# Performance work log

Measured on AMD Instinct MI355X. Metric: run time of the kernel, lower is better.

## Reference

```python
import jax, jax.numpy as jnp
import numpy as np

N_NODES = 50000
N_EDGES = 600000
D = 128


def setup_inputs() -> dict:
    key = jax.random.key(0)
    ks = jax.random.split(key, 10)
    feat = jax.random.normal(ks[0], (N_NODES, D), dtype=jnp.float32)
    edge_src = jax.random.randint(ks[1], (N_EDGES,), 0, N_NODES, dtype=jnp.int64)
    edge_dst = jax.random.randint(ks[2], (N_EDGES,), 0, N_NODES, dtype=jnp.int64)
    edge_w = jax.random.uniform(ks[3], (N_EDGES,), dtype=jnp.float32)
    s = 1.0 / np.sqrt(D)
    W1 = jax.random.uniform(ks[4], (D, D), minval=-s, maxval=s, dtype=jnp.float32)
    W2 = jax.random.uniform(ks[5], (D, D), minval=-s, maxval=s, dtype=jnp.float32)
    # torch GRUCell params: weight_ih [3H, 2D], weight_hh [3H, H], biases [3H]
    W_ih = jax.random.uniform(ks[6], (3 * D, 2 * D), minval=-s, maxval=s, dtype=jnp.float32)
    W_hh = jax.random.uniform(ks[7], (3 * D, D), minval=-s, maxval=s, dtype=jnp.float32)
    b_ih = jax.random.uniform(ks[8], (3 * D,), minval=-s, maxval=s, dtype=jnp.float32)
    b_hh = jax.random.uniform(ks[9], (3 * D,), minval=-s, maxval=s, dtype=jnp.float32)
    return {"feat": feat, "edge_src": edge_src, "edge_dst": edge_dst, "edge_w": edge_w,
            "W1": W1, "W2": W2, "W_ih": W_ih, "W_hh": W_hh, "b_ih": b_ih, "b_hh": b_hh}


def _weighted_mean_agg(feat, w, src, dst, n_nodes):
    # message: ft[src] * w; reduce: sum(m) / sum(w) per dst node (zero for isolated nodes)
    m = feat[src] * w[:, None]                                   # [E, D]
    sm = jax.ops.segment_sum(m, dst, num_segments=n_nodes)      # [N, D]
    sw = jax.ops.segment_sum(w, dst, num_segments=n_nodes)      # [N]
    has = sw > 0
    denom = jnp.where(has, sw, 1.0)[:, None]
    return jnp.where(has[:, None], sm / denom, 0.0)


def reference(feat, edge_src, edge_dst, edge_w, W1, W2, W_ih, W_hh, b_ih, b_hh):
    n = feat.shape[0]
    neigh1 = _weighted_mean_agg(feat, edge_w, edge_src, edge_dst, n)  # forward graph
    neigh2 = _weighted_mean_agg(feat, edge_w, edge_dst, edge_src, n)  # reverse graph
    hn = jnp.concatenate([neigh1 @ W1.T, neigh2 @ W2.T], axis=1)      # [N, 2D]
    # torch.nn.GRUCell(hn, feat)
    gi = hn @ W_ih.T + b_ih    # [N, 3D]
    gh = feat @ W_hh.T + b_hh  # [N, 3D]
    ir, iz, inn = jnp.split(gi, 3, axis=1)
    hr, hz, hnn = jnp.split(gh, 3, axis=1)
    r = jax.nn.sigmoid(ir + hr)
    z = jax.nn.sigmoid(iz + hz)
    ng = jnp.tanh(inn + r * hnn)
    return (1.0 - z) * ng + z * feat
```

## Files before the change

kernel.cpp:

```cpp
#include <hip/hip_runtime.h>
#include <math.h>

#define N_NODES 50000
#define N_EDGES 600000
#define D 128
#define KTOT 384
#define NCOLS 512

#define SCAN_CHUNK 512
#define SCAN_NB ((N_NODES + SCAN_CHUNK - 1) / SCAN_CHUNK)

#define GEMM_ROWB ((N_NODES + 127) / 128)
#define GEMM_NWG  (GEMM_ROWB * 8)
#define NXCD 8
#define KHALF 192

#define BSHIFT 10
#define NBUCKETS ((N_NODES + (1 << BSHIFT) - 1) >> BSHIFT)
#define PA_NB 512
#define PA_CHUNK ((N_EDGES + PA_NB - 1) / PA_NB)
#define PB_SPLIT 4

typedef unsigned int u32;
typedef unsigned short u16;

typedef __attribute__((ext_vector_type(8))) short bf16x8;
typedef __attribute__((ext_vector_type(4))) float f32x4;

__device__ __forceinline__ float bits2f(u32 u) {
    float f; __builtin_memcpy(&f, &u, 4);
    return f;
}
__device__ __forceinline__ u16 f2b(float f) {
    u32 u; __builtin_memcpy(&u, &f, 4);
    u32 r = (u + 0x7fffu + ((u >> 16) & 1u)) >> 16;
    return (u16)r;
}

__global__ void fill_sentinel(float* __restrict__ p, long n, float v) {
    long i = (long)blockIdx.x * blockDim.x + threadIdx.x;
    long stride = (long)gridDim.x * blockDim.x;
    for (; i < n; i += stride) p[i] = v;
}

__global__ void front(const float* __restrict__ feat, u16* __restrict__ fb16,
                      u32* __restrict__ offz) {
    long stride = (long)gridDim.x * blockDim.x;
    long t0 = (long)blockIdx.x * blockDim.x + threadIdx.x;
    for (long i = t0; i < 2 * N_NODES; i += stride) offz[i] = 0u;
    for (long i = t0; i < (long)N_NODES * (D / 4); i += stride) {
        int n = (int)(i >> 5), j4 = (int)(i & 31);
        float4 v = *(const float4*)(feat + (size_t)n * D + j4 * 4);
        ushort4 o;
        o.x = f2b(v.x); o.y = f2b(v.y); o.z = f2b(v.z); o.w = f2b(v.w);
        *(ushort4*)(fb16 + ((size_t)n << 7) + j4 * 4) = o;
    }
}

__global__ void count_both(const int* __restrict__ esrc, const int* __restrict__ edst,
                           int* __restrict__ cnt1, int* __restrict__ cnt2) {
    int e = blockIdx.x * blockDim.x + threadIdx.x;
    if (e < N_EDGES) {
        atomicAdd(&cnt1[edst[e]], 1);
        atomicAdd(&cnt2[esrc[e]], 1);
    }
}

__global__ void scan_partial(const int* __restrict__ off, int* __restrict__ bsum) {
    int dir = blockIdx.y, bx = blockIdx.x, t = threadIdx.x;
    const int* a = off + (size_t)dir * N_NODES;
    int i0 = bx * SCAN_CHUNK + 2 * t;
    int s = 0;
    if (i0 < N_NODES) s += a[i0];
    if (i0 + 1 < N_NODES) s += a[i0 + 1];
    __shared__ int red[256];
    red[t] = s;
    __syncthreads();
    for (int d = 128; d > 0; d >>= 1) {
        if (t < d) red[t] += red[t + d];
        __syncthreads();
    }
    if (t == 0) bsum[dir * SCAN_NB + bx] = red[0];
}

__global__ void scan_bsums(int* __restrict__ bsum) {
    __shared__ int part[256];
    int t = threadIdx.x;
    int i = t & 127, dir = t >> 7;
    int v = (i < SCAN_NB) ? bsum[dir * SCAN_NB + i] : 0;
    part[t] = v;
    __syncthreads();
    for (int d = 1; d < 128; d <<= 1) {
        int add = (i >= d) ? part[t - d] : 0;
        __syncthreads();
        part[t] += add;
        __syncthreads();
    }
    if (i < SCAN_NB) bsum[dir * SCAN_NB + i] = part[t] - v;
}

__global__ void scan_final(int* __restrict__ off, const int* __restrict__ bsum) {
    int dir = blockIdx.y, bx = blockIdx.x, t = threadIdx.x;
    int* a = off + (size_t)dir * N_NODES;
    int base = bsum[dir * SCAN_NB + bx];
    int i0 = bx * SCAN_CHUNK + 2 * t;
    int e0 = (i0 < N_NODES) ? a[i0] : 0;
    int e1 = (i0 + 1 < N_NODES) ? a[i0 + 1] : 0;
    __shared__ int part[256];
    int v = e0 + e1;
    part[t] = v;
    __syncthreads();
    for (int d = 1; d < 256; d <<= 1) {
        int add = (t >= d) ? part[t - d] : 0;
        __syncthreads();
        part[t] += add;
        __syncthreads();
    }
    int tb = base + part[t] - v;
    if (i0 < N_NODES) a[i0] = tb;
    if (i0 + 1 < N_NODES) a[i0 + 1] = tb + e0;
}

__global__ void init_buckets(const int* __restrict__ off1, const int* __restrict__ off2,
                             int* __restrict__ bks) {
    int t = threadIdx.x;
    if (t <= NBUCKETS) {
        int n = t << BSHIFT;
        int s1 = (t == NBUCKETS) ? N_EDGES : off1[n];
        int s2 = (t == NBUCKETS) ? N_EDGES : off2[n];
        bks[t] = s1;
        bks[128 + t] = s2;
        if (t < NBUCKETS) { bks[64 + t] = s1; bks[192 + t] = s2; }
    }
}

__global__ __launch_bounds__(256)
void partA(const int* __restrict__ esrc, const int* __restrict__ edst,
           const float* __restrict__ ew, int* __restrict__ bks,
           uint2* __restrict__ tmp1, uint2* __restrict__ tmp2) {
    __shared__ int lcnt[NBUCKETS];
    __shared__ int lbase[NBUCKETS + 1];
    __shared__ int gbase[NBUCKETS];
    __shared__ uint2 stage[PA_CHUNK];
    int dir = blockIdx.y;
    const int* key = dir ? esrc : edst;
    const int* nbr = dir ? edst : esrc;
    int* bucketFill = bks + (dir ? 192 : 64);
    uint2* tmp = dir ? tmp2 : tmp1;

    int t = threadIdx.x;
    int e0 = blockIdx.x * PA_CHUNK;
    int e1 = min(e0 + PA_CHUNK, N_EDGES);
    if (t < NBUCKETS) lcnt[t] = 0;
    __syncthreads();
    for (int e = e0 + t; e < e1; e += 256)
        atomicAdd(&lcnt[key[e] >> BSHIFT], 1);
    __syncthreads();
    if (t == 0) {
        int s = 0;
        for (int b = 0; b < NBUCKETS; ++b) { lbase[b] = s; s += lcnt[b]; }
        lbase[NBUCKETS] = s;
    }
    __syncthreads();
    if (t < NBUCKETS) {
        gbase[t] = atomicAdd(&bucketFill[t], lcnt[t]);
        lcnt[t] = 0;
    }
    __syncthreads();
    for (int e = e0 + t; e < e1; e += 256) {
        int k = key[e];
        int b = k >> BSHIFT;
        int i = lbase[b] + atomicAdd(&lcnt[b], 1);
        u32 wb = (u32)f2b(ew[e]);
        stage[i] = make_uint2(((u32)k << 16) | (u32)nbr[e], ((u32)b << 16) | wb);
    }
    __syncthreads();
    int total = lbase[NBUCKETS];
    for (int i = t; i < total; i += 256) {
        uint2 v = stage[i];
        int b = (int)(v.y >> 16);
        tmp[gbase[b] + (i - lbase[b])] = make_uint2(v.x, v.y & 0xffffu);
    }
}

__global__ __launch_bounds__(256)
void partB(const uint2* __restrict__ tmp1, const uint2* __restrict__ tmp2,
           const int* __restrict__ bks,
           int* __restrict__ off1, int* __restrict__ off2,
           u32* __restrict__ csr1, u32* __restrict__ csr2) {
    int dir = blockIdx.z;
    const uint2* tmp = dir ? tmp2 : tmp1;
    const int* bucketStart = bks + dir * 128;
    int* off = dir ? off2 : off1;
    u32* csr = dir ? csr2 : csr1;

    int b = blockIdx.x;
    int s = bucketStart[b], e = bucketStart[b + 1];
    int cnt = e - s;
    int per = (cnt + PB_SPLIT - 1) / PB_SPLIT;
    int ss = s + blockIdx.y * per;
    int ee = min(ss + per, e);
    for (int i = ss + (int)threadIdx.x; i < ee; i += 256) {
        uint2 v = tmp[i];
        int dst = v.x >> 16;
        int p = atomicAdd(&off[dst], 1);
        csr[p] = ((v.x & 0xffffu) << 16) | (v.y & 0xffffu);
    }
}

__global__ void gather_both(u16* __restrict__ Ah2, const u16* __restrict__ fb16,
                            const int* __restrict__ off1, const u32* __restrict__ csr1,
                            const int* __restrict__ off2, const u32* __restrict__ csr2) {
    int gw = (blockIdx.x * blockDim.x + threadIdx.x) >> 6;
    int lane = threadIdx.x & 63;
    if (gw >= 2 * N_NODES) return;
    int dir = (gw >= N_NODES);
    int n = dir ? gw - N_NODES : gw;
    const int* off = dir ? off2 : off1;
    const u32* csr = dir ? csr2 : csr1;
    int start = (n == 0) ? 0 : off[n - 1];
    int end = off[n];
    int half = lane >> 5;
    int hl = lane & 31;
    const u16* fbl = fb16 + hl * 4;
    float a0 = 0.f, a1 = 0.f, a2 = 0.f, a3 = 0.f, sw = 0.f;
    int p = start;
    for (; p + 3 < end; p += 4) {
        u32 cA = csr[p + half];
        u32 cB = csr[p + 2 + half];
        uint2 vA = *(const uint2*)(fbl + ((size_t)(cA >> 16) << 7));
        uint2 vB = *(const uint2*)(fbl + ((size_t)(cB >> 16) << 7));
        float wA = bits2f(cA << 16), wB = bits2f(cB << 16);
        a0 += bits2f(vA.x << 16) * wA + bits2f(vB.x << 16) * wB;
        a1 += bits2f(vA.x & 0xffff0000u) * wA + bits2f(vB.x & 0xffff0000u) * wB;
        a2 += bits2f(vA.y << 16) * wA + bits2f(vB.y << 16) * wB;
        a3 += bits2f(vA.y & 0xffff0000u) * wA + bits2f(vB.y & 0xffff0000u) * wB;
        sw += wA + wB;
    }
    for (; p < end; p += 2) {
        u32 c = (p + half < end) ? csr[p + half] : 0u;
        uint2 v = *(const uint2*)(fbl + ((size_t)(c >> 16) << 7));
        float w = bits2f(c << 16);
        a0 += bits2f(v.x << 16) * w;
        a1 += bits2f(v.x & 0xffff0000u) * w;
        a2 += bits2f(v.y << 16) * w;
        a3 += bits2f(v.y & 0xffff0000u) * w;
        sw += w;
    }
    a0 += __shfl_xor(a0, 32);
    a1 += __shfl_xor(a1, 32);
    a2 += __shfl_xor(a2, 32);
    a3 += __shfl_xor(a3, 32);
    sw += __shfl_xor(sw, 32);
    if (lane < 32) {
        float inv = (sw > 0.f) ? 1.f / sw : 0.f;
        if (!isfinite(inv)) inv = 0.f;
        uint2 o;
        o.x = ((u32)f2b(a1 * inv) << 16) | (u32)f2b(a0 * inv);
        o.y = ((u32)f2b(a3 * inv) << 16) | (u32)f2b(a2 * inv);
        *(uint2*)(Ah2 + ((size_t)n << 8) + dir * 128 + hl * 4) = o;
    }
}

__global__ void compute_M(const float* __restrict__ W_ih,
                          const float* __restrict__ W1,
                          const float* __restrict__ W2,
                          float* __restrict__ M1, float* __restrict__ M2) {
    int r = blockIdx.x;
    int k = threadIdx.x;
    int which = blockIdx.y;
    const float* Wsel = which ? W2 : W1;
    const float* ih = W_ih + (size_t)r * (2 * D) + which * D;
    float acc = 0.f;
    for (int j = 0; j < D; ++j) acc += ih[j] * Wsel[j * D + k];
    (which ? M2 : M1)[r * D + k] = acc;
}

__global__ void fill_Bt(const float* __restrict__ M1, const float* __restrict__ M2,
                        const float* __restrict__ W_hh, u16* __restrict__ Bt) {
    int idx = blockIdx.x * blockDim.x + threadIdx.x;
    if (idx >= NCOLS * KTOT) return;
    int cp = idx / KTOT;
    int k  = idx - cp * KTOT;
    int c = cp >> 2, g = cp & 3;
    float v = 0.f;
    if (g <= 1) {
        int r = c + (g == 1 ? 128 : 0);
        v = (k < 128) ? M1[r * D + k]
          : (k < 256) ? M2[r * D + (k - 128)]
                      : W_hh[r * D + (k - 256)];
    } else if (g == 2) {
        int r = c + 256;
        v = (k < 128) ? M1[r * D + k]
          : (k < 256) ? M2[r * D + (k - 128)] : 0.f;
    } else {
        v = (k >= 256) ? W_hh[(c + 256) * D + (k - 256)] : 0.f;
    }
    if (!isfinite(v)) v = 0.f;
    Bt[idx] = f2b(v);
}

#define LOAD_A(m, k) ((k) < 8 ? *(const bf16x8*)(aP[m] + (k) * 32) \
                              : *(const bf16x8*)(fP[m] + ((k) - 8) * 32))

__global__ __launch_bounds__(256)
void gemm_gru_mfma(const u16* __restrict__ Ah2, const u16* __restrict__ fb16,
                   const u16* __restrict__ Bt, const float* __restrict__ feat,
                   const float* __restrict__ b_ih, const float* __restrict__ b_hh,
                   float* __restrict__ out) {
    __shared__ __align__(16) char smem[64 * KHALF * 2];
    float (*epi)[16][65] = (float(*)[16][65])smem;

    int bid = blockIdx.x;
    int wgid = (bid % NXCD) * (GEMM_NWG / NXCD) + bid / NXCD;
    int rowp = wgid >> 3;
    int colb = wgid & 7;
    int tid = threadIdx.x, lane = tid & 63, wid = tid >> 6;
    int mw = rowp * 128 + wid * 32;
    int nw = colb * 64;
    int rif = lane & 15, kg = lane >> 4;

    int scol = tid >> 2;
    int sq   = tid & 3;
    u32 sbase = (u32)scol * (KHALF * 2) + (u32)sq * 96;
    u32 sxor  = (u32)((scol & 7) << 4);
    const u16* ssrc0 = Bt + (size_t)(nw + scol) * KTOT + sq * 48;

    u32 bCol[4], bXor[4];
    #pragma unroll
    for (int n = 0; n < 4; ++n) {
        u32 col = n * 16 + rif;
        bCol[n] = col * (KHALF * 2) + kg * 16;
        bXor[n] = (col & 7) << 4;
    }

    f32x4 acc[2][4];
    #pragma unroll
    for (int m = 0; m < 2; ++m)
        #pragma unroll
        for (int n = 0; n < 4; ++n)
            acc[m][n] = (f32x4){0.f, 0.f, 0.f, 0.f};

    const u16* aP[2];
    const u16* fP[2];
    #pragma unroll
    for (int m = 0; m < 2; ++m) {
        int arow = min(mw + m * 16 + rif, N_NODES - 1);
        aP[m] = Ah2 + ((size_t)arow << 8) + kg * 8;
        fP[m] = fb16 + ((size_t)arow << 7) + kg * 8;
    }

    #pragma unroll
    for (int i = 0; i < 6; ++i) {
        bf16x8 v = *(const bf16x8*)(ssrc0 + i * 8);
        *(bf16x8*)(smem + ((sbase + i * 16) ^ sxor)) = v;
    }

    bf16x8 abuf[4][2];
    #pragma unroll
    for (int s = 0; s < 3; ++s)
        #pragma unroll
        for (int m = 0; m < 2; ++m)
            abuf[s][m] = LOAD_A(m, s);

    __syncthreads();

    #pragma unroll
    for (int ks = 0; ks < 6; ++ks) {
        if (ks + 3 < KTOT / 32) {
            #pragma unroll
            for (int m = 0; m < 2; ++m)
                abuf[(ks + 3) & 3][m] = LOAD_A(m, ks + 3);
        }
        bf16x8 bfr[4];
        #pragma unroll
        for (int n = 0; n < 4; ++n)
            bfr[n] = *(const bf16x8*)(smem + ((bCol[n] + ks * 64) ^ bXor[n]));
        #pragma unroll
        for (int m = 0; m < 2; ++m)
            #pragma unroll
            for (int n = 0; n < 4; ++n)
                acc[m][n] = __builtin_amdgcn_mfma_f32_16x16x32_bf16(
                    abuf[ks & 3][m], bfr[n], acc[m][n], 0, 0, 0);
    }

    __syncthreads();

    #pragma unroll
    for (int i = 0; i < 6; ++i) {
        bf16x8 v = *(const bf16x8*)(ssrc0 + KHALF + i * 8);
        *(bf16x8*)(smem + ((sbase + i * 16) ^ sxor)) = v;
    }
    __syncthreads();

    #pragma unroll
    for (int ks = 6; ks < 12; ++ks) {
        if (ks + 3 < KTOT / 32) {
            #pragma unroll
            for (int m = 0; m < 2; ++m)
                abuf[(ks + 3) & 3][m] = LOAD_A(m, ks + 3);
        }
        bf16x8 bfr[4];
        #pragma unroll
        for (int n = 0; n < 4; ++n)
            bfr[n] = *(const bf16x8*)(smem + ((bCol[n] + (ks - 6) * 64) ^ bXor[n]));
        #pragma unroll
        for (int m = 0; m < 2; ++m)
            #pragma unroll
            for (int n = 0; n < 4; ++n)
                acc[m][n] = __builtin_amdgcn_mfma_f32_16x16x32_bf16(
                    abuf[ks & 3][m], bfr[n], acc[m][n], 0, 0, 0);
    }

    int rc0 = nw >> 2;
    int erow = lane >> 2;
    int g4 = lane & 3;
    int cbase = rc0 + g4 * 4;
    float4 bi_r = *(const float4*)(b_ih + cbase);
    float4 bh_r = *(const float4*)(b_hh + cbase);
    float4 bi_z = *(const float4*)(b_ih + cbase + 128);
    float4 bh_z = *(const float4*)(b_hh + cbase + 128);
    float4 bi_n = *(const float4*)(b_ih + cbase + 256);
    float4 bh_n = *(const float4*)(b_hh + cbase + 256);

    #pragma unroll
    for (int m = 0; m < 2; ++m) {
        __syncthreads();
        #pragma unroll
        for (int n = 0; n < 4; ++n)
            #pragma unroll
            for (int reg = 0; reg < 4; ++reg)
                epi[wid][kg * 4 + reg][n * 16 + rif] = acc[m][n][reg];
        __syncthreads();

        float4 q0 = *(const float4*)&epi[wid][erow][g4 * 16 + 0];
        float4 q1 = *(const float4*)&epi[wid][erow][g4 * 16 + 4];
        float4 q2 = *(const float4*)&epi[wid][erow][g4 * 16 + 8];
        float4 q3 = *(const float4*)&epi[wid][erow][g4 * 16 + 12];

        int node = mw + m * 16 + erow;
        if (node < N_NODES) {
            float4 f = *(const float4*)(feat + (size_t)node * D + cbase);
            float4 res;
            {
                float r = 1.f / (1.f + __expf(-(q0.x + bi_r.x + bh_r.x)));
                float z = 1.f / (1.f + __expf(-(q0.y + bi_z.x + bh_z.x)));
                float ng = tanhf(q0.z + bi_n.x + r * (q0.w + bh_n.x));
                res.x = (1.f - z) * ng + z * f.x;
            }
            {
                float r = 1.f / (1.f + __expf(-(q1.x + bi_r.y + bh_r.y)));
                float z = 1.f / (1.f + __expf(-(q1.y + bi_z.y + bh_z.y)));
                float ng = tanhf(q1.z + bi_n.y + r * (q1.w + bh_n.y));
                res.y = (1.f - z) * ng + z * f.y;
            }
            {
                float r = 1.f / (1.f + __expf(-(q2.x + bi_r.z + bh_r.z)));
                float z = 1.f / (1.f + __expf(-(q2.y + bi_z.z + bh_z.z)));
                float ng = tanhf(q2.z + bi_n.z + r * (q2.w + bh_n.z));
                res.z = (1.f - z) * ng + z * f.z;
            }
            {
                float r = 1.f / (1.f + __expf(-(q3.x + bi_r.w + bh_r.w)));
                float z = 1.f / (1.f + __expf(-(q3.y + bi_z.w + bh_z.w)));
                float ng = tanhf(q3.z + bi_n.w + r * (q3.w + bh_n.w));
                res.w = (1.f - z) * ng + z * f.w;
            }
            *(float4*)(out + (size_t)node * D + cbase) = res;
        }
    }
}

extern "C" void kernel_launch(void* const* d_in, const int* in_sizes, int n_in,
                              void* d_out, int out_size, void* d_ws, size_t ws_size,
                              hipStream_t stream) {
    const float* feat = (const float*)d_in[0];
    const int*   esrc = (const int*)d_in[1];
    const int*   edst = (const int*)d_in[2];
    const float* ew   = (const float*)d_in[3];
    const float* W1   = (const float*)d_in[4];
    const float* W2   = (const float*)d_in[5];
    const float* W_ih = (const float*)d_in[6];
    const float* W_hh = (const float*)d_in[7];
    const float* b_ih = (const float*)d_in[8];
    const float* b_hh = (const float*)d_in[9];
    float* out = (float*)d_out;

    const size_t AH2_ELEMS = (size_t)N_NODES * 256;
    const size_t FB_ELEMS  = (size_t)N_NODES * 128;
    const size_t needWords = (AH2_ELEMS + FB_ELEMS) / 2 + 2 * N_NODES
                           + 2 * (size_t)N_EDGES
                           + 4 * (size_t)N_EDGES
                           + 512 + 2 * (size_t)KTOT * D + (NCOLS * KTOT) / 2;
    if (ws_size < needWords * 4) {
        fill_sentinel<<<512, 256, 0, stream>>>(out, (long)out_size, 12345.0f);
        return;
    }

    u16*   Ah2  = (u16*)d_ws;
    u16*   fb16 = Ah2 + AH2_ELEMS;
    int*   off1 = (int*)(fb16 + FB_ELEMS);
    int*   off2 = off1 + N_NODES;
    u32*   csr1 = (u32*)(off2 + N_NODES);
    u32*   csr2 = csr1 + N_EDGES;
    uint2* tmp1 = (uint2*)(csr2 + N_EDGES);
    uint2* tmp2 = tmp1 + N_EDGES;
    int*   bsum = (int*)(tmp2 + N_EDGES);
    int*   bks  = bsum + 256;
    float* M1   = (float*)(bks + 256);
    float* M2   = M1 + KTOT * D;
    u16*   Bt   = (u16*)(M2 + KTOT * D);

    const int EB = (N_EDGES + 255) / 256;

    front<<<2048, 256, 0, stream>>>(feat, fb16, (u32*)off1);
    count_both<<<EB, 256, 0, stream>>>(esrc, edst, off1, off2);
    scan_partial<<<dim3(SCAN_NB, 2), 256, 0, stream>>>(off1, bsum);
    scan_bsums<<<1, 256, 0, stream>>>(bsum);
    scan_final<<<dim3(SCAN_NB, 2), 256, 0, stream>>>(off1, bsum);

    init_buckets<<<1, 64, 0, stream>>>(off1, off2, bks);
    partA<<<dim3(PA_NB, 2), 256, 0, stream>>>(esrc, edst, ew, bks, tmp1, tmp2);
    partB<<<dim3(NBUCKETS, PB_SPLIT, 2), 256, 0, stream>>>(
        tmp1, tmp2, bks, off1, off2, csr1, csr2);

    gather_both<<<(2 * N_NODES * 64 + 255) / 256, 256, 0, stream>>>(
        Ah2, fb16, off1, csr1, off2, csr2);

    compute_M<<<dim3(KTOT, 2), 128, 0, stream>>>(W_ih, W1, W2, M1, M2);
    fill_Bt<<<(NCOLS * KTOT + 255) / 256, 256, 0, stream>>>(M1, M2, W_hh, Bt);

    gemm_gru_mfma<<<GEMM_NWG, 256, 0, stream>>>(Ah2, fb16, Bt, feat, b_ih, b_hh, out);
}
```

Before: 249.6 us.

## Replace three-pass scan with decoupled lookback scan; unroll gather by eight

Merges the three-kernel exclusive scan over node degrees into one single-pass kernel that uses decoupled lookback flags, with the flags zeroed in the front kernel. This removes two kernel launches and their dependency gaps. The gather kernel gets an 8-edge unrolled loop to keep more independent loads in flight, and its block size drops to 128 threads. The lookback spin-waits rely on earlier blocks being scheduled first, which holds for about 98 blocks per direction, and the wider unroll raises register use.

Result: slower. 261.9 us (+4.9%).

```diff
diff --git a/kernel.cpp b/kernel.cpp
--- a/kernel.cpp
+++ b/kernel.cpp
@@ -44,10 +44,11 @@
 }
 
 __global__ void front(const float* __restrict__ feat, u16* __restrict__ fb16,
-                      u32* __restrict__ offz) {
+                      u32* __restrict__ offz, u32* __restrict__ flagz) {
     long stride = (long)gridDim.x * blockDim.x;
     long t0 = (long)blockIdx.x * blockDim.x + threadIdx.x;
     for (long i = t0; i < 2 * N_NODES; i += stride) offz[i] = 0u;
+    for (long i = t0; i < 256; i += stride) flagz[i] = 0u;
     for (long i = t0; i < (long)N_NODES * (D / 4); i += stride) {
         int n = (int)(i >> 5), j4 = (int)(i & 31);
         float4 v = *(const float4*)(feat + (size_t)n * D + j4 * 4);
@@ -66,47 +67,16 @@
     }
 }
 
-__global__ void scan_partial(const int* __restrict__ off, int* __restrict__ bsum) {
-    int dir = blockIdx.y, bx = blockIdx.x, t = threadIdx.x;
-    const int* a = off + (size_t)dir * N_NODES;
-    int i0 = bx * SCAN_CHUNK + 2 * t;
-    int s = 0;
-    if (i0 < N_NODES) s += a[i0];
-    if (i0 + 1 < N_NODES) s += a[i0 + 1];
-    __shared__ int red[256];
-    red[t] = s;
-    __syncthreads();
-    for (int d = 128; d > 0; d >>= 1) {
-        if (t < d) red[t] += red[t + d];
-        __syncthreads();
-    }
-    if (t == 0) bsum[dir * SCAN_NB + bx] = red[0];
-}
-
-__global__ void scan_bsums(int* __restrict__ bsum) {
-    __shared__ int part[256];
-    int t = threadIdx.x;
-    int i = t & 127, dir = t >> 7;
-    int v = (i < SCAN_NB) ? bsum[dir * SCAN_NB + i] : 0;
-    part[t] = v;
-    __syncthreads();
-    for (int d = 1; d < 128; d <<= 1) {
-        int add = (i >= d) ? part[t - d] : 0;
-        __syncthreads();
-        part[t] += add;
-        __syncthreads();
-    }
-    if (i < SCAN_NB) bsum[dir * SCAN_NB + i] = part[t] - v;
-}
-
-__global__ void scan_final(int* __restrict__ off, const int* __restrict__ bsum) {
+__global__ __launch_bounds__(256)
+void scan_lookback(int* __restrict__ off, u32* __restrict__ flags) {
     int dir = blockIdx.y, bx = blockIdx.x, t = threadIdx.x;
     int* a = off + (size_t)dir * N_NODES;
-    int base = bsum[dir * SCAN_NB + bx];
+    u32* flag = flags + dir * 128;
     int i0 = bx * SCAN_CHUNK + 2 * t;
     int e0 = (i0 < N_NODES) ? a[i0] : 0;
     int e1 = (i0 + 1 < N_NODES) ? a[i0 + 1] : 0;
     __shared__ int part[256];
+    __shared__ int sbase;
     int v = e0 + e1;
     part[t] = v;
     __syncthreads();
@@ -116,7 +86,33 @@
         part[t] += add;
         __syncthreads();
     }
-    int tb = base + part[t] - v;
+    int total = part[255];
+    if (t == 0) {
+        if (bx == 0) {
+            __hip_atomic_store(&flag[0], (2u << 30) | (u32)total,
+                               __ATOMIC_RELEASE, __HIP_MEMORY_SCOPE_AGENT);
+            sbase = 0;
+        } else {
+            __hip_atomic_store(&flag[bx], (1u << 30) | (u32)total,
+                               __ATOMIC_RELEASE, __HIP_MEMORY_SCOPE_AGENT);
+            int run = 0, j = bx - 1;
+            while (true) {
+                u32 f;
+                do {
+                    f = __hip_atomic_load(&flag[j], __ATOMIC_ACQUIRE,
+                                          __HIP_MEMORY_SCOPE_AGENT);
+                } while ((f >> 30) == 0u);
+                run += (int)(f & 0x3fffffffu);
+                if ((f >> 30) == 2u) break;
+                --j;
+            }
+            __hip_atomic_store(&flag[bx], (2u << 30) | (u32)(run + total),
+                               __ATOMIC_RELEASE, __HIP_MEMORY_SCOPE_AGENT);
+            sbase = run;
+        }
+    }
+    __syncthreads();
+    int tb = sbase + part[t] - v;
     if (i0 < N_NODES) a[i0] = tb;
     if (i0 + 1 < N_NODES) a[i0 + 1] = tb + e0;
 }
@@ -208,9 +204,10 @@
     }
 }
 
-__global__ void gather_both(u16* __restrict__ Ah2, const u16* __restrict__ fb16,
-                            const int* __restrict__ off1, const u32* __restrict__ csr1,
-                            const int* __restrict__ off2, const u32* __restrict__ csr2) {
+__global__ __launch_bounds__(128)
+void gather_both(u16* __restrict__ Ah2, const u16* __restrict__ fb16,
+                 const int* __restrict__ off1, const u32* __restrict__ csr1,
+                 const int* __restrict__ off2, const u32* __restrict__ csr2) {
     int gw = (blockIdx.x * blockDim.x + threadIdx.x) >> 6;
     int lane = threadIdx.x & 63;
     if (gw >= 2 * N_NODES) return;
@@ -225,9 +222,27 @@
     const u16* fbl = fb16 + hl * 4;
     float a0 = 0.f, a1 = 0.f, a2 = 0.f, a3 = 0.f, sw = 0.f;
     int p = start;
+    for (; p + 7 < end; p += 8) {
+        u32 cA = csr[p + half],     cB = csr[p + 2 + half];
+        u32 cC = csr[p + 4 + half], cD = csr[p + 6 + half];
+        uint2 vA = *(const uint2*)(fbl + ((size_t)(cA >> 16) << 7));
+        uint2 vB = *(const uint2*)(fbl + ((size_t)(cB >> 16) << 7));
+        uint2 vC = *(const uint2*)(fbl + ((size_t)(cC >> 16) << 7));
+        uint2 vD = *(const uint2*)(fbl + ((size_t)(cD >> 16) << 7));
+        float wA = bits2f(cA << 16), wB = bits2f(cB << 16);
+        float wC = bits2f(cC << 16), wD = bits2f(cD << 16);
+        a0 += bits2f(vA.x << 16) * wA + bits2f(vB.x << 16) * wB
+            + bits2f(vC.x << 16) * wC + bits2f(vD.x << 16) * wD;
+        a1 += bits2f(vA.x & 0xffff0000u) * wA + bits2f(vB.x & 0xffff0000u) * wB
+            + bits2f(vC.x & 0xffff0000u) * wC + bits2f(vD.x & 0xffff0000u) * wD;
+        a2 += bits2f(vA.y << 16) * wA + bits2f(vB.y << 16) * wB
+            + bits2f(vC.y << 16) * wC + bits2f(vD.y << 16) * wD;
+        a3 += bits2f(vA.y & 0xffff0000u) * wA + bits2f(vB.y & 0xffff0000u) * wB
+            + bits2f(vC.y & 0xffff0000u) * wC + bits2f(vD.y & 0xffff0000u) * wD;
+        sw += wA + wB + wC + wD;
+    }
     for (; p + 3 < end; p += 4) {
-        u32 cA = csr[p + half];
-        u32 cB = csr[p + 2 + half];
+        u32 cA = csr[p + half], cB = csr[p + 2 + half];
         uint2 vA = *(const uint2*)(fbl + ((size_t)(cA >> 16) << 7));
         uint2 vB = *(const uint2*)(fbl + ((size_t)(cB >> 16) << 7));
         float wA = bits2f(cA << 16), wB = bits2f(cB << 16);
@@ -505,26 +520,24 @@
     u32*   csr2 = csr1 + N_EDGES;
     uint2* tmp1 = (uint2*)(csr2 + N_EDGES);
     uint2* tmp2 = tmp1 + N_EDGES;
-    int*   bsum = (int*)(tmp2 + N_EDGES);
-    int*   bks  = bsum + 256;
+    u32*   flags = (u32*)(tmp2 + N_EDGES);
+    int*   bks  = (int*)(flags + 256);
     float* M1   = (float*)(bks + 256);
     float* M2   = M1 + KTOT * D;
     u16*   Bt   = (u16*)(M2 + KTOT * D);
 
     const int EB = (N_EDGES + 255) / 256;
 
-    front<<<2048, 256, 0, stream>>>(feat, fb16, (u32*)off1);
+    front<<<2048, 256, 0, stream>>>(feat, fb16, (u32*)off1, flags);
     count_both<<<EB, 256, 0, stream>>>(esrc, edst, off1, off2);
-    scan_partial<<<dim3(SCAN_NB, 2), 256, 0, stream>>>(off1, bsum);
-    scan_bsums<<<1, 256, 0, stream>>>(bsum);
-    scan_final<<<dim3(SCAN_NB, 2), 256, 0, stream>>>(off1, bsum);
+    scan_lookback<<<dim3(SCAN_NB, 2), 256, 0, stream>>>(off1, flags);
 
     init_buckets<<<1, 64, 0, stream>>>(off1, off2, bks);
     partA<<<dim3(PA_NB, 2), 256, 0, stream>>>(esrc, edst, ew, bks, tmp1, tmp2);
     partB<<<dim3(NBUCKETS, PB_SPLIT, 2), 256, 0, stream>>>(
         tmp1, tmp2, bks, off1, off2, csr1, csr2);
 
-    gather_both<<<(2 * N_NODES * 64 + 255) / 256, 256, 0, stream>>>(
+    gather_both<<<(2 * N_NODES * 64 + 127) / 128, 128, 0, stream>>>(
         Ah2, fb16, off1, csr1, off2, csr2);
 
     compute_M<<<dim3(KTOT, 2), 128, 0, stream>>>(W_ih, W1, W2, M1, M2);
```

## Use shared-memory per-bucket counters in CSR fill and unroll gather by eight

Applied to the files above, without the earlier changes.

partB now gives each bucket to a single block. The block loads that bucket's node offsets into shared memory and places edges with LDS atomics, where before it used global atomics on the offset array. Because off is no longer advanced in place, gather reads start as off[n] and end as off[n+1]. The gather loop also gets an 8-edge unrolled stage for more loads in flight and runs with 128-thread blocks. The cost is fewer partB blocks, so less parallelism on large buckets.

Result: faster. 208.6 us (-16.4%).

```diff
diff --git a/kernel.cpp b/kernel.cpp
--- a/kernel.cpp
+++ b/kernel.cpp
@@ -16,10 +16,10 @@
 #define KHALF 192
 
 #define BSHIFT 10
-#define NBUCKETS ((N_NODES + (1 << BSHIFT) - 1) >> BSHIFT)
+#define BSIZE (1 << BSHIFT)
+#define NBUCKETS ((N_NODES + BSIZE - 1) >> BSHIFT)
 #define PA_NB 512
 #define PA_CHUNK ((N_EDGES + PA_NB - 1) / PA_NB)
-#define PB_SPLIT 4
 
 typedef unsigned int u32;
 typedef unsigned short u16;
@@ -186,31 +186,37 @@
 __global__ __launch_bounds__(256)
 void partB(const uint2* __restrict__ tmp1, const uint2* __restrict__ tmp2,
            const int* __restrict__ bks,
-           int* __restrict__ off1, int* __restrict__ off2,
+           const int* __restrict__ off1, const int* __restrict__ off2,
            u32* __restrict__ csr1, u32* __restrict__ csr2) {
-    int dir = blockIdx.z;
+    __shared__ int lcnt[BSIZE];
+    __shared__ int loff[BSIZE];
+    int dir = blockIdx.y;
     const uint2* tmp = dir ? tmp2 : tmp1;
     const int* bucketStart = bks + dir * 128;
-    int* off = dir ? off2 : off1;
+    const int* off = dir ? off2 : off1;
     u32* csr = dir ? csr2 : csr1;
 
     int b = blockIdx.x;
     int s = bucketStart[b], e = bucketStart[b + 1];
-    int cnt = e - s;
-    int per = (cnt + PB_SPLIT - 1) / PB_SPLIT;
-    int ss = s + blockIdx.y * per;
-    int ee = min(ss + per, e);
-    for (int i = ss + (int)threadIdx.x; i < ee; i += 256) {
+    int nbase = b << BSHIFT;
+    for (int i = threadIdx.x; i < BSIZE; i += 256) {
+        lcnt[i] = 0;
+        int nn = nbase + i;
+        loff[i] = (nn < N_NODES) ? off[nn] : 0;
+    }
+    __syncthreads();
+    for (int i = s + (int)threadIdx.x; i < e; i += 256) {
         uint2 v = tmp[i];
-        int dst = v.x >> 16;
-        int p = atomicAdd(&off[dst], 1);
+        int li = (v.x >> 16) & (BSIZE - 1);
+        int p = loff[li] + atomicAdd(&lcnt[li], 1);
         csr[p] = ((v.x & 0xffffu) << 16) | (v.y & 0xffffu);
     }
 }
 
-__global__ void gather_both(u16* __restrict__ Ah2, const u16* __restrict__ fb16,
-                            const int* __restrict__ off1, const u32* __restrict__ csr1,
-                            const int* __restrict__ off2, const u32* __restrict__ csr2) {
+__global__ __launch_bounds__(128)
+void gather_both(u16* __restrict__ Ah2, const u16* __restrict__ fb16,
+                 const int* __restrict__ off1, const u32* __restrict__ csr1,
+                 const int* __restrict__ off2, const u32* __restrict__ csr2) {
     int gw = (blockIdx.x * blockDim.x + threadIdx.x) >> 6;
     int lane = threadIdx.x & 63;
     if (gw >= 2 * N_NODES) return;
@@ -218,16 +224,34 @@
     int n = dir ? gw - N_NODES : gw;
     const int* off = dir ? off2 : off1;
     const u32* csr = dir ? csr2 : csr1;
-    int start = (n == 0) ? 0 : off[n - 1];
-    int end = off[n];
+    int start = off[n];
+    int end = (n + 1 < N_NODES) ? off[n + 1] : N_EDGES;
     int half = lane >> 5;
     int hl = lane & 31;
     const u16* fbl = fb16 + hl * 4;
     float a0 = 0.f, a1 = 0.f, a2 = 0.f, a3 = 0.f, sw = 0.f;
     int p = start;
+    for (; p + 7 < end; p += 8) {
+        u32 cA = csr[p + half],     cB = csr[p + 2 + half];
+        u32 cC = csr[p + 4 + half], cD = csr[p + 6 + half];
+        uint2 vA = *(const uint2*)(fbl + ((size_t)(cA >> 16) << 7));
+        uint2 vB = *(const uint2*)(fbl + ((size_t)(cB >> 16) << 7));
+        uint2 vC = *(const uint2*)(fbl + ((size_t)(cC >> 16) << 7));
+        uint2 vD = *(const uint2*)(fbl + ((size_t)(cD >> 16) << 7));
+        float wA = bits2f(cA << 16), wB = bits2f(cB << 16);
+        float wC = bits2f(cC << 16), wD = bits2f(cD << 16);
+        a0 += bits2f(vA.x << 16) * wA + bits2f(vB.x << 16) * wB
+            + bits2f(vC.x << 16) * wC + bits2f(vD.x << 16) * wD;
+        a1 += bits2f(vA.x & 0xffff0000u) * wA + bits2f(vB.x & 0xffff0000u) * wB
+            + bits2f(vC.x & 0xffff0000u) * wC + bits2f(vD.x & 0xffff0000u) * wD;
+        a2 += bits2f(vA.y << 16) * wA + bits2f(vB.y << 16) * wB
+            + bits2f(vC.y << 16) * wC + bits2f(vD.y << 16) * wD;
+        a3 += bits2f(vA.y & 0xffff0000u) * wA + bits2f(vB.y & 0xffff0000u) * wB
+            + bits2f(vC.y & 0xffff0000u) * wC + bits2f(vD.y & 0xffff0000u) * wD;
+        sw += wA + wB + wC + wD;
+    }
     for (; p + 3 < end; p += 4) {
-        u32 cA = csr[p + half];
-        u32 cB = csr[p + 2 + half];
+        u32 cA = csr[p + half], cB = csr[p + 2 + half];
         uint2 vA = *(const uint2*)(fbl + ((size_t)(cA >> 16) << 7));
         uint2 vB = *(const uint2*)(fbl + ((size_t)(cB >> 16) << 7));
         float wA = bits2f(cA << 16), wB = bits2f(cB << 16);
@@ -521,10 +545,10 @@
 
     init_buckets<<<1, 64, 0, stream>>>(off1, off2, bks);
     partA<<<dim3(PA_NB, 2), 256, 0, stream>>>(esrc, edst, ew, bks, tmp1, tmp2);
-    partB<<<dim3(NBUCKETS, PB_SPLIT, 2), 256, 0, stream>>>(
+    partB<<<dim3(NBUCKETS, 2), 256, 0, stream>>>(
         tmp1, tmp2, bks, off1, off2, csr1, csr2);
 
-    gather_both<<<(2 * N_NODES * 64 + 255) / 256, 256, 0, stream>>>(
+    gather_both<<<(2 * N_NODES * 64 + 127) / 128, 128, 0, stream>>>(
         Ah2, fb16, off1, csr1, off2, csr2);
 
     compute_M<<<dim3(KTOT, 2), 128, 0, stream>>>(W_ih, W1, W2, M1, M2);
```
